# Performance work log

Hardware: AMD Instinct MI355X
Metric: run time of the kernel (lower is better)

## Reference

```python
import jax, jax.numpy as jnp
import numpy as np

N_NODES = 50000
N_EDGES = 800000
IN_FEAT = 128
HIDDEN = 256
OUT = 64


def setup_inputs() -> dict:
    key = jax.random.key(0)
    ks = jax.random.split(key, 8)
    x = jax.random.normal(ks[0], (N_NODES, IN_FEAT), dtype=jnp.float32)
    edge_index = jax.random.randint(ks[1], (2, N_EDGES), 0, N_NODES, dtype=jnp.int64)
    s1 = 1.0 / np.sqrt(IN_FEAT)
    s2 = 1.0 / np.sqrt(HIDDEN)
    W1_l = jax.random.uniform(ks[2], (HIDDEN, IN_FEAT), jnp.float32, -s1, s1)
    W1_r = jax.random.uniform(ks[3], (HIDDEN, IN_FEAT), jnp.float32, -s1, s1)
    b1 = jax.random.uniform(ks[4], (HIDDEN,), jnp.float32, -s1, s1)
    W2_l = jax.random.uniform(ks[5], (OUT, HIDDEN), jnp.float32, -s2, s2)
    W2_r = jax.random.uniform(ks[6], (OUT, HIDDEN), jnp.float32, -s2, s2)
    b2 = jax.random.uniform(ks[7], (OUT,), jnp.float32, -s2, s2)
    return {"x": x, "edge_index": edge_index, "W1_l": W1_l, "W1_r": W1_r,
            "b1": b1, "W2_l": W2_l, "W2_r": W2_r, "b2": b2}


def _sage_conv(x, src, dst, W_l, W_r, b):
    # mean aggregation of source features onto destination nodes
    msgs = x[src]                                                   # [E, F]
    agg = jax.ops.segment_sum(msgs, dst, num_segments=N_NODES)      # [N, F]
    cnt = jax.ops.segment_sum(jnp.ones((src.shape[0], 1), x.dtype), dst,
                              num_segments=N_NODES)                 # [N, 1]
    agg = agg / jnp.maximum(cnt, 1.0)
    # out = lin_l(agg) + lin_r(x); bias only on lin_l (PyG SAGEConv)
    return agg @ W_l.T + b + x @ W_r.T


def reference(x, edge_index, W1_l, W1_r, b1, W2_l, W2_r, b2):
    src, dst = edge_index[0], edge_index[1]
    h = jax.nn.relu(_sage_conv(x, src, dst, W1_l, W1_r, b1))
    # dropout is identity in eval mode
    return _sage_conv(h, src, dst, W2_l, W2_r, b2)
```

## Files before the change

### kernel.cpp

```cpp
#include <hip/hip_runtime.h>
#include <hip/hip_bf16.h>

#define N_NODES 50000
#define N_EDGES 800000
#define IN_FEAT 128
#define HIDDEN  256
#define OUT_F   64
#define M_PAD   50048
#define CONV_NB 1024
#define GATH_NB 2048
#define NGROUPS 12500
#define BSH     7
#define NBUCK   391
#define NCHUNK  256
#define BCAP    4096

typedef __attribute__((ext_vector_type(8))) short short8;
typedef __attribute__((ext_vector_type(4))) float f32x4;

static __device__ __forceinline__ unsigned short f2bf(float f) {
    unsigned u = __float_as_uint(f);
    unsigned r = (u + 0x7fffu + ((u >> 16) & 1u)) >> 16;
    return (unsigned short)r;
}
static __device__ __forceinline__ float bflo(unsigned u) { return __uint_as_float(u << 16); }
static __device__ __forceinline__ float bfhi(unsigned u) { return __uint_as_float(u & 0xffff0000u); }

__global__ __launch_bounds__(256) void bhcp_k(const int* __restrict__ dst,
                                              int* __restrict__ bh,
                                              const float* __restrict__ x,
                                              unsigned int* __restrict__ A1u,
                                              const float* __restrict__ W1l,
                                              const float* __restrict__ W1r,
                                              unsigned int* __restrict__ Wf1,
                                              const float* __restrict__ W2l,
                                              const float* __restrict__ W2r,
                                              unsigned int* __restrict__ Wf2) {
    __shared__ int hist[NBUCK];
    int b = blockIdx.x, t = threadIdx.x;
    if (b < NCHUNK) {
        for (int i = t; i < NBUCK; i += 256) hist[i] = 0;
        __syncthreads();
        for (int e = b * 256 + t; e < N_EDGES; e += NCHUNK * 256)
            atomicAdd(&hist[dst[e] >> BSH], 1);
        __syncthreads();
        for (int i = t; i < NBUCK; i += 256) bh[b * NBUCK + i] = hist[i];
    } else if (b < NCHUNK + CONV_NB) {
        const int T = CONV_NB * 256;
        for (int i = (b - NCHUNK) * 256 + t; i < N_NODES * 64; i += T) {
            int n = i >> 6, p = i & 63;
            float2 v = ((const float2*)(x + (size_t)n * IN_FEAT))[p];
            A1u[(size_t)n * 128 + 64 + p] = (unsigned)f2bf(v.x) | ((unsigned)f2bf(v.y) << 16);
        }
    } else if (b < NCHUNK + CONV_NB + 128) {
        int i = (b - NCHUNK - CONV_NB) * 256 + t;
        int s = i * 2;
        int j = s & 7, lane = (s >> 3) & 63, nt = (s >> 9) & 15, ks = s >> 13;
        int n = nt * 16 + (lane & 15);
        int k = ks * 32 + ((lane >> 4) << 3) + j;
        float v0, v1;
        if (k < 128) { v0 = W1l[n * 128 + k];       v1 = W1l[n * 128 + k + 1]; }
        else         { v0 = W1r[n * 128 + k - 128]; v1 = W1r[n * 128 + k - 127]; }
        Wf1[i] = (unsigned)f2bf(v0) | ((unsigned)f2bf(v1) << 16);
    } else {
        int i = (b - NCHUNK - CONV_NB - 128) * 256 + t;
        int s = i * 2;
        int j = s & 7, lane = (s >> 3) & 63, nt = (s >> 9) & 7, ks = s >> 12;
        int n = nt * 16 + (lane & 15);
        int k = ks * 32 + ((lane >> 4) << 3) + j;
        float v0, v1;
        if (n < 64) { v0 = W2l[n * 256 + k];        v1 = W2l[n * 256 + k + 1]; }
        else        { v0 = W2r[(n - 64) * 256 + k]; v1 = W2r[(n - 64) * 256 + k + 1]; }
        Wf2[i] = (unsigned)f2bf(v0) | ((unsigned)f2bf(v1) << 16);
    }
}

__global__ __launch_bounds__(256) void chunkscan_k(const int* __restrict__ bh,
                                                   int* __restrict__ obuf,
                                                   int* __restrict__ btot) {
    __shared__ int s[256];
    int q = blockIdx.x, t = threadIdx.x;
    int v = bh[t * NBUCK + q];
    s[t] = v;
    __syncthreads();
    for (int off = 1; off < 256; off <<= 1) {
        int add = (t >= off) ? s[t - off] : 0;
        __syncthreads();
        s[t] += add;
        __syncthreads();
    }
    obuf[t * NBUCK + q] = s[t] - v;
    if (t == 255) btot[q] = s[255];
}

__global__ __launch_bounds__(512) void bucketscan_k(const int* __restrict__ btot,
                                                    int* __restrict__ bbase,
                                                    int* __restrict__ rowptr) {
    __shared__ int s[512];
    int t = threadIdx.x;
    int v = (t < NBUCK) ? btot[t] : 0;
    s[t] = v;
    __syncthreads();
    for (int off = 1; off < 512; off <<= 1) {
        int add = (t >= off) ? s[t - off] : 0;
        __syncthreads();
        s[t] += add;
        __syncthreads();
    }
    if (t < NBUCK) bbase[t] = s[t] - v;
    if (t == 0) { bbase[NBUCK] = N_EDGES; rowptr[N_NODES] = N_EDGES; }
}

__global__ __launch_bounds__(256) void reorder_k(const int* __restrict__ dst,
                                                 const int* __restrict__ src,
                                                 const int* __restrict__ bbase,
                                                 const int* __restrict__ obuf,
                                                 int2* __restrict__ ebuf) {
    __shared__ int cur[NBUCK];
    int b = blockIdx.x, t = threadIdx.x;
    for (int i = t; i < NBUCK; i += 256) cur[i] = bbase[i] + obuf[b * NBUCK + i];
    __syncthreads();
    for (int e = b * 256 + t; e < N_EDGES; e += NCHUNK * 256) {
        int d = dst[e], sv = src[e];
        int pos = atomicAdd(&cur[d >> BSH], 1);
        ebuf[pos] = make_int2(sv, d);
    }
}

__global__ __launch_bounds__(256) void bucketcsr_k(const int2* __restrict__ ebuf,
                                                   const int* __restrict__ bbase,
                                                   int* __restrict__ rowptr,
                                                   int* __restrict__ eids) {
    __shared__ int2 ed[BCAP];
    __shared__ int cnt[128];
    __shared__ int s[256];
    __shared__ int cur[128];
    int b = blockIdx.x, t = threadIdx.x;
    int e0 = bbase[b], e1 = bbase[b + 1];
    int m = e1 - e0; if (m > BCAP) m = BCAP;
    int d0 = b << BSH;
    if (t < 128) cnt[t] = 0;
    for (int i = t; i < m; i += 256) ed[i] = ebuf[e0 + i];
    __syncthreads();
    for (int i = t; i < m; i += 256) atomicAdd(&cnt[ed[i].y - d0], 1);
    __syncthreads();
    s[t] = (t < 128) ? cnt[t] : 0;
    __syncthreads();
    for (int off = 1; off < 256; off <<= 1) {
        int add = (t >= off) ? s[t - off] : 0;
        __syncthreads();
        s[t] += add;
        __syncthreads();
    }
    if (t < 128) {
        int excl = s[t] - cnt[t];
        cur[t] = excl;
        int node = d0 + t;
        if (node < N_NODES) rowptr[node] = e0 + excl;
    }
    __syncthreads();
    for (int i = t; i < m; i += 256) {
        int pos = atomicAdd(&cur[ed[i].y - d0], 1);
        eids[e0 + pos] = ed[i].x;
    }
}

__global__ __launch_bounds__(256) void gather1_k(const unsigned int* __restrict__ Au,
                                                 const int* __restrict__ eids,
                                                 const int* __restrict__ rowptr,
                                                 unsigned int* __restrict__ Aw) {
    int w = threadIdx.x >> 6, lane = threadIdx.x & 63;
    int eg = lane >> 4, cq = lane & 15;
    for (int g = blockIdx.x; g < NGROUPS; g += GATH_NB) {
        int node = g * 4 + w;
        int b = rowptr[node], e = rowptr[node + 1];
        float a0 = 0.f, a1 = 0.f, a2 = 0.f, a3 = 0.f, a4 = 0.f, a5 = 0.f, a6 = 0.f, a7 = 0.f;
        int i = b + eg;
        for (; i + 12 < e; i += 16) {
            int s0 = eids[i], s1 = eids[i + 4], s2 = eids[i + 8], s3 = eids[i + 12];
            uint4 v0 = ((const uint4*)(Au + (size_t)s0 * 128 + 64))[cq];
            uint4 v1 = ((const uint4*)(Au + (size_t)s1 * 128 + 64))[cq];
            uint4 v2 = ((const uint4*)(Au + (size_t)s2 * 128 + 64))[cq];
            uint4 v3 = ((const uint4*)(Au + (size_t)s3 * 128 + 64))[cq];
            a0 += bflo(v0.x) + bflo(v1.x) + bflo(v2.x) + bflo(v3.x);
            a1 += bfhi(v0.x) + bfhi(v1.x) + bfhi(v2.x) + bfhi(v3.x);
            a2 += bflo(v0.y) + bflo(v1.y) + bflo(v2.y) + bflo(v3.y);
            a3 += bfhi(v0.y) + bfhi(v1.y) + bfhi(v2.y) + bfhi(v3.y);
            a4 += bflo(v0.z) + bflo(v1.z) + bflo(v2.z) + bflo(v3.z);
            a5 += bfhi(v0.z) + bfhi(v1.z) + bfhi(v2.z) + bfhi(v3.z);
            a6 += bflo(v0.w) + bflo(v1.w) + bflo(v2.w) + bflo(v3.w);
            a7 += bfhi(v0.w) + bfhi(v1.w) + bfhi(v2.w) + bfhi(v3.w);
        }
        for (; i < e; i += 4) {
            int s = eids[i];
            uint4 v = ((const uint4*)(Au + (size_t)s * 128 + 64))[cq];
            a0 += bflo(v.x); a1 += bfhi(v.x);
            a2 += bflo(v.y); a3 += bfhi(v.y);
            a4 += bflo(v.z); a5 += bfhi(v.z);
            a6 += bflo(v.w); a7 += bfhi(v.w);
        }
#pragma unroll
        for (int m = 16; m <= 32; m <<= 1) {
            a0 += __shfl_xor(a0, m); a1 += __shfl_xor(a1, m);
            a2 += __shfl_xor(a2, m); a3 += __shfl_xor(a3, m);
            a4 += __shfl_xor(a4, m); a5 += __shfl_xor(a5, m);
            a6 += __shfl_xor(a6, m); a7 += __shfl_xor(a7, m);
        }
        if (eg == 0) {
            int deg = e - b; if (deg < 1) deg = 1;
            float inv = 1.f / (float)deg;
            uint4 r;
            r.x = (unsigned)f2bf(a0 * inv) | ((unsigned)f2bf(a1 * inv) << 16);
            r.y = (unsigned)f2bf(a2 * inv) | ((unsigned)f2bf(a3 * inv) << 16);
            r.z = (unsigned)f2bf(a4 * inv) | ((unsigned)f2bf(a5 * inv) << 16);
            r.w = (unsigned)f2bf(a6 * inv) | ((unsigned)f2bf(a7 * inv) << 16);
            ((uint4*)(Aw + (size_t)node * 128))[cq] = r;
        }
    }
}

__global__ __launch_bounds__(256) void mfma_gemm1_k(
        const unsigned short* __restrict__ A, const unsigned short* __restrict__ Wf,
        const float* __restrict__ b1, unsigned short* __restrict__ h) {
    int wv = threadIdx.x >> 6, lane = threadIdx.x & 63;
    int rowh = wv >> 1, colh = wv & 1;
    int m0 = blockIdx.x * 64 + rowh * 32;
    int row = lane & 15, kg = lane >> 4;
    const short8* Wf8 = (const short8*)Wf;

    short8 af[2][8];
#pragma unroll
    for (int mt = 0; mt < 2; mt++) {
        const short8* ar = (const short8*)(A + (size_t)(m0 + mt * 16 + row) * 256 + kg * 8);
#pragma unroll
        for (int ks = 0; ks < 8; ks++) af[mt][ks] = ar[ks * 4];
    }
    f32x4 acc[2][8];
#pragma unroll
    for (int mt = 0; mt < 2; mt++)
#pragma unroll
        for (int nt = 0; nt < 8; nt++) acc[mt][nt] = (f32x4)(0.f);

#pragma unroll
    for (int ks = 0; ks < 8; ks++) {
        short8 bf[8];
#pragma unroll
        for (int nt = 0; nt < 8; nt++)
            bf[nt] = Wf8[(ks * 16 + colh * 8 + nt) * 64 + lane];
#pragma unroll
        for (int nt = 0; nt < 8; nt++) {
#pragma unroll
            for (int mt = 0; mt < 2; mt++)
                acc[mt][nt] = __builtin_amdgcn_mfma_f32_16x16x32_bf16(af[mt][ks], bf[nt],
                                                                      acc[mt][nt], 0, 0, 0);
        }
    }

#pragma unroll
    for (int mt = 0; mt < 2; mt++) {
        int r0 = m0 + mt * 16 + kg * 4;
#pragma unroll
        for (int nt = 0; nt < 8; nt++) {
            int c = colh * 128 + nt * 16 + row;
            float bias = b1[c];
#pragma unroll
            for (int i = 0; i < 4; i++) {
                float v = acc[mt][nt][i] + bias;
                v = v > 0.f ? v : 0.f;
                h[(size_t)(r0 + i) * 256 + c] = f2bf(v);
            }
        }
    }
}

__global__ __launch_bounds__(256) void mfma_gemm2_k(
        const unsigned short* __restrict__ A, const unsigned short* __restrict__ Wf,
        const float* __restrict__ b2, unsigned short* __restrict__ y,
        float* __restrict__ out) {
    int wv = threadIdx.x >> 6, lane = threadIdx.x & 63;
    int m0 = blockIdx.x * 128 + wv * 32;
    int row = lane & 15, kg = lane >> 4;
    const short8* Wf8 = (const short8*)Wf;

    short8 af[2][8];
#pragma unroll
    for (int mt = 0; mt < 2; mt++) {
        const short8* ar = (const short8*)(A + (size_t)(m0 + mt * 16 + row) * 256 + kg * 8);
#pragma unroll
        for (int ks = 0; ks < 8; ks++) af[mt][ks] = ar[ks * 4];
    }
    f32x4 acc[2][8];
#pragma unroll
    for (int mt = 0; mt < 2; mt++)
#pragma unroll
        for (int nt = 0; nt < 8; nt++) acc[mt][nt] = (f32x4)(0.f);

#pragma unroll
    for (int ks = 0; ks < 8; ks++) {
        short8 bf[8];
#pragma unroll
        for (int nt = 0; nt < 8; nt++)
            bf[nt] = Wf8[(ks * 8 + nt) * 64 + lane];
#pragma unroll
        for (int nt = 0; nt < 8; nt++) {
#pragma unroll
            for (int mt = 0; mt < 2; mt++)
                acc[mt][nt] = __builtin_amdgcn_mfma_f32_16x16x32_bf16(af[mt][ks], bf[nt],
                                                                      acc[mt][nt], 0, 0, 0);
        }
    }

#pragma unroll
    for (int mt = 0; mt < 2; mt++) {
        int r0 = m0 + mt * 16 + kg * 4;
#pragma unroll
        for (int nt = 0; nt < 8; nt++) {
            int c = nt * 16 + row;
#pragma unroll
            for (int i = 0; i < 4; i++) {
                int rr = r0 + i;
                if (nt < 4) {
                    y[(size_t)rr * OUT_F + c] = f2bf(acc[mt][nt][i]);
                } else if (rr < N_NODES) {
                    out[(size_t)rr * OUT_F + (c - 64)] = acc[mt][nt][i] + b2[c - 64];
                }
            }
        }
    }
}

__global__ __launch_bounds__(256) void gather2_k(const unsigned int* __restrict__ yu,
                                                 const int* __restrict__ eids,
                                                 const int* __restrict__ rowptr,
                                                 float* __restrict__ out) {
    int w = threadIdx.x >> 6, lane = threadIdx.x & 63;
    int eg = lane >> 3, cq = lane & 7;
    for (int g = blockIdx.x; g < NGROUPS; g += GATH_NB) {
        int node = g * 4 + w;
        int b = rowptr[node], e = rowptr[node + 1];
        float a0 = 0.f, a1 = 0.f, a2 = 0.f, a3 = 0.f, a4 = 0.f, a5 = 0.f, a6 = 0.f, a7 = 0.f;
        int i = b + eg;
        for (; i + 8 < e; i += 16) {
            int s0 = eids[i], s1 = eids[i + 8];
            uint4 v0 = ((const uint4*)(yu + (size_t)s0 * 32))[cq];
            uint4 v1 = ((const uint4*)(yu + (size_t)s1 * 32))[cq];
            a0 += bflo(v0.x) + bflo(v1.x); a1 += bfhi(v0.x) + bfhi(v1.x);
            a2 += bflo(v0.y) + bflo(v1.y); a3 += bfhi(v0.y) + bfhi(v1.y);
            a4 += bflo(v0.z) + bflo(v1.z); a5 += bfhi(v0.z) + bfhi(v1.z);
            a6 += bflo(v0.w) + bflo(v1.w); a7 += bfhi(v0.w) + bfhi(v1.w);
        }
        for (; i < e; i += 8) {
            int s = eids[i];
            uint4 v = ((const uint4*)(yu + (size_t)s * 32))[cq];
            a0 += bflo(v.x); a1 += bfhi(v.x);
            a2 += bflo(v.y); a3 += bfhi(v.y);
            a4 += bflo(v.z); a5 += bfhi(v.z);
            a6 += bflo(v.w); a7 += bfhi(v.w);
        }
#pragma unroll
        for (int m = 8; m <= 32; m <<= 1) {
            a0 += __shfl_xor(a0, m); a1 += __shfl_xor(a1, m);
            a2 += __shfl_xor(a2, m); a3 += __shfl_xor(a3, m);
            a4 += __shfl_xor(a4, m); a5 += __shfl_xor(a5, m);
            a6 += __shfl_xor(a6, m); a7 += __shfl_xor(a7, m);
        }
        if (eg == 0) {
            int deg = e - b; if (deg < 1) deg = 1;
            float inv = 1.f / (float)deg;
            float4* p = (float4*)(out + (size_t)node * OUT_F + cq * 8);
            float4 c0 = p[0], c1 = p[1];
            c0.x += a0 * inv; c0.y += a1 * inv; c0.z += a2 * inv; c0.w += a3 * inv;
            c1.x += a4 * inv; c1.y += a5 * inv; c1.z += a6 * inv; c1.w += a7 * inv;
            p[0] = c0; p[1] = c1;
        }
    }
}

extern "C" void kernel_launch(void* const* d_in, const int* in_sizes, int n_in,
                              void* d_out, int out_size, void* d_ws, size_t ws_size,
                              hipStream_t stream) {
    const float* x    = (const float*)d_in[0];
    const int*   eidx = (const int*)d_in[1];
    const float* W1l  = (const float*)d_in[2];
    const float* W1r  = (const float*)d_in[3];
    const float* b1   = (const float*)d_in[4];
    const float* W2l  = (const float*)d_in[5];
    const float* W2r  = (const float*)d_in[6];
    const float* b2   = (const float*)d_in[7];
    float* out = (float*)d_out;

    const int* src = eidx;
    const int* dst = eidx + N_EDGES;

    unsigned short* A1   = (unsigned short*)d_ws;
    unsigned short* hbuf = A1 + (size_t)M_PAD * 256;
    unsigned short* ybuf = hbuf + (size_t)M_PAD * 256;
    unsigned short* W1f  = ybuf + (size_t)M_PAD * OUT_F;
    unsigned short* W2f  = W1f + 65536;
    int2* ebuf  = (int2*)(W2f + 32768);
    int* rowptr = (int*)(ebuf + N_EDGES);
    int* eids   = rowptr + N_NODES + 1;
    int* bh     = eids + N_EDGES;
    int* obuf   = bh + NCHUNK * NBUCK;
    int* btot   = obuf + NCHUNK * NBUCK;
    int* bbase  = btot + NBUCK;

    bhcp_k<<<NCHUNK + CONV_NB + 192, 256, 0, stream>>>(dst, bh, x, (unsigned int*)A1,
                                                       W1l, W1r, (unsigned int*)W1f,
                                                       W2l, W2r, (unsigned int*)W2f);

    chunkscan_k<<<NBUCK, 256, 0, stream>>>(bh, obuf, btot);
    bucketscan_k<<<1, 512, 0, stream>>>(btot, bbase, rowptr);
    reorder_k<<<NCHUNK, 256, 0, stream>>>(dst, src, bbase, obuf, ebuf);
    bucketcsr_k<<<NBUCK, 256, 0, stream>>>(ebuf, bbase, rowptr, eids);

    gather1_k<<<GATH_NB, 256, 0, stream>>>((const unsigned int*)A1, eids, rowptr,
                                           (unsigned int*)A1);

    mfma_gemm1_k<<<M_PAD / 64, 256, 0, stream>>>(A1, W1f, b1, hbuf);

    mfma_gemm2_k<<<M_PAD / 128, 256, 0, stream>>>(hbuf, W2f, b2, ybuf, out);

    gather2_k<<<GATH_NB, 256, 0, stream>>>((const unsigned int*)ybuf, eids, rowptr, out);
}
```

Baseline: 130.9 us.

## Replace scan-based bucket sort with fixed-capacity buckets and global atomic cursors

Removes the two prefix-scan kernels and the separate histogram pass. Each reorder block now builds its own histogram and reserves space in fixed-capacity per-bucket slots through global atomics, and bucketcsr derives rowptr plus per-node degree from those slots. Gathers read the degree instead of rowptr[node+1], and the x-to-bf16 conversion now uses float4 loads. Edges beyond a bucket's capacity are silently dropped, and edge order within a bucket becomes nondeterministic.

```diff
diff --git a/kernel.cpp b/kernel.cpp
--- a/kernel.cpp
+++ b/kernel.cpp
@@ -26,34 +26,29 @@
 static __device__ __forceinline__ float bflo(unsigned u) { return __uint_as_float(u << 16); }
 static __device__ __forceinline__ float bfhi(unsigned u) { return __uint_as_float(u & 0xffff0000u); }
 
-__global__ __launch_bounds__(256) void bhcp_k(const int* __restrict__ dst,
-                                              int* __restrict__ bh,
-                                              const float* __restrict__ x,
+__global__ __launch_bounds__(256) void prep_k(const float* __restrict__ x,
                                               unsigned int* __restrict__ A1u,
                                               const float* __restrict__ W1l,
                                               const float* __restrict__ W1r,
                                               unsigned int* __restrict__ Wf1,
                                               const float* __restrict__ W2l,
                                               const float* __restrict__ W2r,
-                                              unsigned int* __restrict__ Wf2) {
-    __shared__ int hist[NBUCK];
+                                              unsigned int* __restrict__ Wf2,
+                                              int* __restrict__ gcur) {
     int b = blockIdx.x, t = threadIdx.x;
-    if (b < NCHUNK) {
-        for (int i = t; i < NBUCK; i += 256) hist[i] = 0;
-        __syncthreads();
-        for (int e = b * 256 + t; e < N_EDGES; e += NCHUNK * 256)
-            atomicAdd(&hist[dst[e] >> BSH], 1);
-        __syncthreads();
-        for (int i = t; i < NBUCK; i += 256) bh[b * NBUCK + i] = hist[i];
-    } else if (b < NCHUNK + CONV_NB) {
+    if (b < CONV_NB) {
         const int T = CONV_NB * 256;
-        for (int i = (b - NCHUNK) * 256 + t; i < N_NODES * 64; i += T) {
-            int n = i >> 6, p = i & 63;
-            float2 v = ((const float2*)(x + (size_t)n * IN_FEAT))[p];
-            A1u[(size_t)n * 128 + 64 + p] = (unsigned)f2bf(v.x) | ((unsigned)f2bf(v.y) << 16);
-        }
-    } else if (b < NCHUNK + CONV_NB + 128) {
-        int i = (b - NCHUNK - CONV_NB) * 256 + t;
+        const float4* X4 = (const float4*)x;
+        for (int i = b * 256 + t; i < N_NODES * 32; i += T) {
+            int n = i >> 5, p4 = i & 31;
+            float4 v = X4[i];
+            unsigned lo = (unsigned)f2bf(v.x) | ((unsigned)f2bf(v.y) << 16);
+            unsigned hi = (unsigned)f2bf(v.z) | ((unsigned)f2bf(v.w) << 16);
+            unsigned int* dstp = A1u + (size_t)n * 128 + 64 + p4 * 2;
+            dstp[0] = lo; dstp[1] = hi;
+        }
+    } else if (b < CONV_NB + 128) {
+        int i = (b - CONV_NB) * 256 + t;
         int s = i * 2;
         int j = s & 7, lane = (s >> 3) & 63, nt = (s >> 9) & 15, ks = s >> 13;
         int n = nt * 16 + (lane & 15);
@@ -62,8 +57,8 @@
         if (k < 128) { v0 = W1l[n * 128 + k];       v1 = W1l[n * 128 + k + 1]; }
         else         { v0 = W1r[n * 128 + k - 128]; v1 = W1r[n * 128 + k - 127]; }
         Wf1[i] = (unsigned)f2bf(v0) | ((unsigned)f2bf(v1) << 16);
-    } else {
-        int i = (b - NCHUNK - CONV_NB - 128) * 256 + t;
+    } else if (b < CONV_NB + 128 + 64) {
+        int i = (b - CONV_NB - 128) * 256 + t;
         int s = i * 2;
         int j = s & 7, lane = (s >> 3) & 63, nt = (s >> 9) & 7, ks = s >> 12;
         int n = nt * 16 + (lane & 15);
@@ -72,72 +67,48 @@
         if (n < 64) { v0 = W2l[n * 256 + k];        v1 = W2l[n * 256 + k + 1]; }
         else        { v0 = W2r[(n - 64) * 256 + k]; v1 = W2r[(n - 64) * 256 + k + 1]; }
         Wf2[i] = (unsigned)f2bf(v0) | ((unsigned)f2bf(v1) << 16);
-    }
-}
-
-__global__ __launch_bounds__(256) void chunkscan_k(const int* __restrict__ bh,
-                                                   int* __restrict__ obuf,
-                                                   int* __restrict__ btot) {
-    __shared__ int s[256];
-    int q = blockIdx.x, t = threadIdx.x;
-    int v = bh[t * NBUCK + q];
-    s[t] = v;
-    __syncthreads();
-    for (int off = 1; off < 256; off <<= 1) {
-        int add = (t >= off) ? s[t - off] : 0;
-        __syncthreads();
-        s[t] += add;
-        __syncthreads();
-    }
-    obuf[t * NBUCK + q] = s[t] - v;
-    if (t == 255) btot[q] = s[255];
-}
-
-__global__ __launch_bounds__(512) void bucketscan_k(const int* __restrict__ btot,
-                                                    int* __restrict__ bbase,
-                                                    int* __restrict__ rowptr) {
-    __shared__ int s[512];
-    int t = threadIdx.x;
-    int v = (t < NBUCK) ? btot[t] : 0;
-    s[t] = v;
-    __syncthreads();
-    for (int off = 1; off < 512; off <<= 1) {
-        int add = (t >= off) ? s[t - off] : 0;
-        __syncthreads();
-        s[t] += add;
-        __syncthreads();
-    }
-    if (t < NBUCK) bbase[t] = s[t] - v;
-    if (t == 0) { bbase[NBUCK] = N_EDGES; rowptr[N_NODES] = N_EDGES; }
-}
-
-__global__ __launch_bounds__(256) void reorder_k(const int* __restrict__ dst,
-                                                 const int* __restrict__ src,
-                                                 const int* __restrict__ bbase,
-                                                 const int* __restrict__ obuf,
-                                                 int2* __restrict__ ebuf) {
+    } else {
+        for (int i = t; i < NBUCK; i += 256) gcur[i] = 0;
+    }
+}
+
+__global__ __launch_bounds__(256) void reorder2_k(const int* __restrict__ dst,
+                                                  const int* __restrict__ src,
+                                                  int* __restrict__ gcur,
+                                                  int2* __restrict__ ebuf) {
+    __shared__ int hist[NBUCK];
     __shared__ int cur[NBUCK];
     int b = blockIdx.x, t = threadIdx.x;
-    for (int i = t; i < NBUCK; i += 256) cur[i] = bbase[i] + obuf[b * NBUCK + i];
+    for (int i = t; i < NBUCK; i += 256) hist[i] = 0;
+    __syncthreads();
+    for (int e = b * 256 + t; e < N_EDGES; e += NCHUNK * 256)
+        atomicAdd(&hist[dst[e] >> BSH], 1);
+    __syncthreads();
+    for (int i = t; i < NBUCK; i += 256) {
+        int h = hist[i];
+        cur[i] = (h > 0) ? atomicAdd(&gcur[i], h) : 0;
+    }
     __syncthreads();
     for (int e = b * 256 + t; e < N_EDGES; e += NCHUNK * 256) {
         int d = dst[e], sv = src[e];
-        int pos = atomicAdd(&cur[d >> BSH], 1);
-        ebuf[pos] = make_int2(sv, d);
+        int q = d >> BSH;
+        int pos = atomicAdd(&cur[q], 1);
+        if (pos < BCAP) ebuf[(size_t)q * BCAP + pos] = make_int2(sv, d);
     }
 }
 
 __global__ __launch_bounds__(256) void bucketcsr_k(const int2* __restrict__ ebuf,
-                                                   const int* __restrict__ bbase,
+                                                   const int* __restrict__ gcur,
                                                    int* __restrict__ rowptr,
+                                                   int* __restrict__ degv,
                                                    int* __restrict__ eids) {
     __shared__ int2 ed[BCAP];
     __shared__ int cnt[128];
     __shared__ int s[256];
     __shared__ int cur[128];
     int b = blockIdx.x, t = threadIdx.x;
-    int e0 = bbase[b], e1 = bbase[b + 1];
-    int m = e1 - e0; if (m > BCAP) m = BCAP;
+    int e0 = b * BCAP;
+    int m = gcur[b]; if (m > BCAP) m = BCAP;
     int d0 = b << BSH;
     if (t < 128) cnt[t] = 0;
     for (int i = t; i < m; i += 256) ed[i] = ebuf[e0 + i];
@@ -156,7 +127,7 @@
         int excl = s[t] - cnt[t];
         cur[t] = excl;
         int node = d0 + t;
-        if (node < N_NODES) rowptr[node] = e0 + excl;
+        if (node < N_NODES) { rowptr[node] = e0 + excl; degv[node] = cnt[t]; }
     }
     __syncthreads();
     for (int i = t; i < m; i += 256) {
@@ -168,12 +139,13 @@
 __global__ __launch_bounds__(256) void gather1_k(const unsigned int* __restrict__ Au,
                                                  const int* __restrict__ eids,
                                                  const int* __restrict__ rowptr,
+                                                 const int* __restrict__ degv,
                                                  unsigned int* __restrict__ Aw) {
     int w = threadIdx.x >> 6, lane = threadIdx.x & 63;
     int eg = lane >> 4, cq = lane & 15;
     for (int g = blockIdx.x; g < NGROUPS; g += GATH_NB) {
         int node = g * 4 + w;
-        int b = rowptr[node], e = rowptr[node + 1];
+        int b = rowptr[node], e = b + degv[node];
         float a0 = 0.f, a1 = 0.f, a2 = 0.f, a3 = 0.f, a4 = 0.f, a5 = 0.f, a6 = 0.f, a7 = 0.f;
         int i = b + eg;
         for (; i + 12 < e; i += 16) {
@@ -332,12 +304,13 @@
 __global__ __launch_bounds__(256) void gather2_k(const unsigned int* __restrict__ yu,
                                                  const int* __restrict__ eids,
                                                  const int* __restrict__ rowptr,
+                                                 const int* __restrict__ degv,
                                                  float* __restrict__ out) {
     int w = threadIdx.x >> 6, lane = threadIdx.x & 63;
     int eg = lane >> 3, cq = lane & 7;
     for (int g = blockIdx.x; g < NGROUPS; g += GATH_NB) {
         int node = g * 4 + w;
-        int b = rowptr[node], e = rowptr[node + 1];
+        int b = rowptr[node], e = b + degv[node];
         float a0 = 0.f, a1 = 0.f, a2 = 0.f, a3 = 0.f, a4 = 0.f, a5 = 0.f, a6 = 0.f, a7 = 0.f;
         int i = b + eg;
         for (; i + 8 < e; i += 16) {
@@ -398,28 +371,25 @@
     unsigned short* W1f  = ybuf + (size_t)M_PAD * OUT_F;
     unsigned short* W2f  = W1f + 65536;
     int2* ebuf  = (int2*)(W2f + 32768);
-    int* rowptr = (int*)(ebuf + N_EDGES);
-    int* eids   = rowptr + N_NODES + 1;
-    int* bh     = eids + N_EDGES;
-    int* obuf   = bh + NCHUNK * NBUCK;
-    int* btot   = obuf + NCHUNK * NBUCK;
-    int* bbase  = btot + NBUCK;
-
-    bhcp_k<<<NCHUNK + CONV_NB + 192, 256, 0, stream>>>(dst, bh, x, (unsigned int*)A1,
+    int* eids   = (int*)(ebuf + (size_t)NBUCK * BCAP);
+    int* rowptr = eids + (size_t)NBUCK * BCAP;
+    int* degv   = rowptr + N_NODES;
+    int* gcur   = degv + N_NODES;
+
+    prep_k<<<CONV_NB + 128 + 64 + 1, 256, 0, stream>>>(x, (unsigned int*)A1,
                                                        W1l, W1r, (unsigned int*)W1f,
-                                                       W2l, W2r, (unsigned int*)W2f);
-
-    chunkscan_k<<<NBUCK, 256, 0, stream>>>(bh, obuf, btot);
-    bucketscan_k<<<1, 512, 0, stream>>>(btot, bbase, rowptr);
-    reorder_k<<<NCHUNK, 256, 0, stream>>>(dst, src, bbase, obuf, ebuf);
-    bucketcsr_k<<<NBUCK, 256, 0, stream>>>(ebuf, bbase, rowptr, eids);
-
-    gather1_k<<<GATH_NB, 256, 0, stream>>>((const unsigned int*)A1, eids, rowptr,
+                                                       W2l, W2r, (unsigned int*)W2f, gcur);
+
+    reorder2_k<<<NCHUNK, 256, 0, stream>>>(dst, src, gcur, ebuf);
+
+    bucketcsr_k<<<NBUCK, 256, 0, stream>>>(ebuf, gcur, rowptr, degv, eids);
+
+    gather1_k<<<GATH_NB, 256, 0, stream>>>((const unsigned int*)A1, eids, rowptr, degv,
                                            (unsigned int*)A1);
 
     mfma_gemm1_k<<<M_PAD / 64, 256, 0, stream>>>(A1, W1f, b1, hbuf);
 
     mfma_gemm2_k<<<M_PAD / 128, 256, 0, stream>>>(hbuf, W2f, b2, ybuf, out);
 
-    gather2_k<<<GATH_NB, 256, 0, stream>>>((const unsigned int*)ybuf, eids, rowptr, out);
-}
+    gather2_k<<<GATH_NB, 256, 0, stream>>>((const unsigned int*)ybuf, eids, rowptr, degv, out);
+}
```

After: 131.6 us. About the same (+0.5%).
